# Performance work log

Hardware: AMD Instinct MI355X
Metric: run time of the kernel (lower is better)

The kernel has to match this reference:

```python
import jax, jax.numpy as jnp
import numpy as np

B, S, D = 1, 2048, 4096
H, KV, HD = 32, 8, 128
C = 4096  # cache length
THETA = 1000000.0
NEG = -1e9


def setup_inputs() -> dict:
    key = jax.random.key(0)
    ks = jax.random.split(key, 8)
    std = 0.02
    x = jax.random.normal(ks[0], (B, S, D), jnp.float32)
    wq = jax.random.normal(ks[1], (H * HD, D), jnp.float32) * std
    wk = jax.random.normal(ks[2], (KV * HD, D), jnp.float32) * std
    wv = jax.random.normal(ks[3], (KV * HD, D), jnp.float32) * std
    wo = jax.random.normal(ks[4], (D, H * HD), jnp.float32) * std
    k_cache = jnp.zeros((B, KV, C, HD), jnp.float32)
    v_cache = jnp.zeros((B, KV, C, HD), jnp.float32)
    # rotary tables (real/imag of freqs_cis)
    inv_freq = 1.0 / (THETA ** (jnp.arange(0, HD, 2, dtype=jnp.float32) / HD))  # [HD/2]
    t = jnp.arange(C, dtype=jnp.float32)
    freqs = jnp.outer(t, inv_freq)  # [C, HD/2]
    cos, sin = jnp.cos(freqs), jnp.sin(freqs)
    # causal additive mask over cache positions
    mask = jnp.where(jnp.tril(jnp.ones((C, C), bool)), 0.0, NEG).astype(jnp.float32)
    storage_idx = jnp.arange(S, dtype=jnp.int32)
    return {"x": x, "wq": wq, "wk": wk, "wv": wv, "wo": wo,
            "k_cache": k_cache, "v_cache": v_cache,
            "cos": cos, "sin": sin, "mask": mask, "storage_idx": storage_idx}


def _rope(x, cos, sin):
    # x: [B, h, S, HD]; cos/sin: [S, HD/2] -> complex mult on interleaved pairs
    xr, xi = x[..., 0::2], x[..., 1::2]
    c = cos[None, None, :, :]
    s = sin[None, None, :, :]
    or_, oi_ = xr * c - xi * s, xr * s + xi * c
    return jnp.stack([or_, oi_], axis=-1).reshape(x.shape)


def reference(x, wq, wk, wv, wo, k_cache, v_cache, cos, sin, mask, storage_idx):
    bsz, seqlen, _ = x.shape
    xq = jnp.einsum('bsd,ed->bse', x, wq).reshape(bsz, seqlen, H, HD).transpose(0, 2, 1, 3)
    xk = jnp.einsum('bsd,ed->bse', x, wk).reshape(bsz, seqlen, KV, HD).transpose(0, 2, 1, 3)
    xv = jnp.einsum('bsd,ed->bse', x, wv).reshape(bsz, seqlen, KV, HD).transpose(0, 2, 1, 3)
    cos_g, sin_g = cos[storage_idx], sin[storage_idx]
    xq = _rope(xq, cos_g, sin_g)
    xk = _rope(xk, cos_g, sin_g)
    # scatter into KV cache at storage_idx along the position axis
    keys = k_cache.at[:, :, storage_idx, :].set(xk)
    values = v_cache.at[:, :, storage_idx, :].set(xv)
    # GQA: repeat kv heads (kv-head-major, matches expand+reshape)
    rep = H // KV
    keys = jnp.repeat(keys, rep, axis=1)      # [B, H, C, HD]
    values = jnp.repeat(values, rep, axis=1)  # [B, H, C, HD]
    scores = jnp.einsum('bhqd,bhkd->bhqk', xq, keys) / np.sqrt(HD)
    scores = scores + mask[storage_idx][None, None, :, :]
    attn = jax.nn.softmax(scores, axis=-1)
    out = jnp.einsum('bhqk,bhkd->bhqd', attn, values)
    out = out.transpose(0, 2, 1, 3).reshape(bsz, seqlen, H * HD)
    return jnp.einsum('bse,de->bsd', out, wo)
```

## Files before the change

kernel.cpp:

```cpp
#include <hip/hip_runtime.h>
#include <cstdint>
#include <cstddef>

#define S_LEN 2048
#define DM    4096
#define NH    32
#define NKV   8
#define HDIM  128
#define EQ    4096
#define EKV   1024
#define SC_LOG2E 0.1275325477889277f

typedef unsigned short u16;
typedef short bf16x8 __attribute__((ext_vector_type(8)));
typedef float f32x4  __attribute__((ext_vector_type(4)));

__device__ __forceinline__ u16 f2bf(float f) {
  union { float f; unsigned u; } v; v.f = f;
  unsigned r = v.u + 0x7FFFu + ((v.u >> 16) & 1u);
  return (u16)(r >> 16);
}
__device__ __forceinline__ float bf2f(u16 b) {
  union { unsigned u; float f; } v; v.u = ((unsigned)b) << 16;
  return v.f;
}
__device__ __forceinline__ void glds16(const void* g, void* l) {
  __builtin_amdgcn_global_load_lds((const __attribute__((address_space(1))) void*)g,
                                   (__attribute__((address_space(3))) void*)l, 16, 0, 0);
}

__global__ void cast_all(const float* __restrict__ x, const float* __restrict__ wq,
                         const float* __restrict__ wk, const float* __restrict__ wv,
                         const float* __restrict__ wo,
                         u16* __restrict__ xb, u16* __restrict__ wqb,
                         u16* __restrict__ wkb, u16* __restrict__ wvb,
                         u16* __restrict__ wob) {
  const size_t stride = (size_t)gridDim.x * blockDim.x;
  for (size_t u = (size_t)blockIdx.x * blockDim.x + threadIdx.x; u < 12582912u; u += stride) {
    const float* in; u16* outp; size_t i;
    if (u < 2097152u)      { in = x;  outp = xb;  i = u; }
    else if (u < 6291456u) { in = wq; outp = wqb; i = u - 2097152u; }
    else if (u < 7340032u) { in = wk; outp = wkb; i = u - 6291456u; }
    else if (u < 8388608u) { in = wv; outp = wvb; i = u - 7340032u; }
    else                   { in = wo; outp = wob; i = u - 8388608u; }
    float4 f = ((const float4*)in)[i];
    ushort4 b;
    b.x = f2bf(f.x); b.y = f2bf(f.y); b.z = f2bf(f.z); b.w = f2bf(f.w);
    ((ushort4*)outp)[i] = b;
  }
}

template<int UN>
__device__ __forceinline__ void stage_t(const u16* __restrict__ g, int ldg, int k0,
                                        u16* ldsp, int t) {
  const int wb = t & ~63;
#pragma unroll
  for (int j = 0; j < UN / 256; ++j) {
    const int U = j * 256 + t;
    const int row = U >> 3, u = U & 7;
    const int uu = u ^ (row & 7);
    glds16(g + (size_t)row * ldg + k0 + uu * 8, ldsp + (size_t)(j * 256 + wb) * 8);
  }
}

template<int NF, bool QKV3>
__global__ __launch_bounds__(256, 2)
void gemm2p(const u16* __restrict__ A, const u16* __restrict__ B,
            void* __restrict__ Cq, u16* __restrict__ Ck, u16* __restrict__ Cv,
            int K) {
  constexpr int BN = 64 * NF;
  constexpr int AT = 128 * 64;
  constexpr int BT = BN * 64;
  __shared__ u16 lds[2 * (AT + BT)];
  const int t = threadIdx.x;
  const int l = t & 63, lr = l & 15, lg = l >> 4;
  const int wid = t >> 6, wm = wid >> 1, wn = wid & 1;
  const int m0 = blockIdx.y * 128, n0 = blockIdx.x * BN;
  const int KT = K >> 6;

  const u16* Ab = A + (size_t)m0 * K;
  const u16* Bb = B + (size_t)n0 * K;

  f32x4 acc[4][2 * NF] = {};

  stage_t<1024>(Ab, K, 0, &lds[0], t);
  stage_t<BT / 8>(Bb, K, 0, &lds[2 * AT], t);
  __syncthreads();

  int cur = 0;
#pragma unroll 1
  for (int tau = 0; tau < KT; ++tau) {
    const int kn = (tau + 1 < KT ? tau + 1 : KT - 1) * 64;
    stage_t<1024>(Ab, K, kn, &lds[(cur ^ 1) * AT], t);
    stage_t<BT / 8>(Bb, K, kn, &lds[2 * AT + (cur ^ 1) * BT], t);

    const int aBase = cur * AT;
    const int bBase = 2 * AT + cur * BT;

    bf16x8 af[4][2];
#pragma unroll
    for (int mf = 0; mf < 4; ++mf)
#pragma unroll
      for (int kk = 0; kk < 2; ++kk) {
        const int row = wm * 64 + mf * 16 + lr;
        const int uu = ((kk * 4 + lg) ^ (row & 7)) * 8;
        af[mf][kk] = *(const bf16x8*)&lds[aBase + row * 64 + uu];
      }

#pragma unroll
    for (int n = 0; n < 2 * NF; ++n) {
      const int brow = wn * (32 * NF) + n * 16 + lr;
      const int u0 = ((0 * 4 + lg) ^ (brow & 7)) * 8;
      const int u1 = ((1 * 4 + lg) ^ (brow & 7)) * 8;
      bf16x8 b0 = *(const bf16x8*)&lds[bBase + brow * 64 + u0];
      bf16x8 b1 = *(const bf16x8*)&lds[bBase + brow * 64 + u1];
#pragma unroll
      for (int mf = 0; mf < 4; ++mf) {
        acc[mf][n] = __builtin_amdgcn_mfma_f32_16x16x32_bf16(af[mf][0], b0, acc[mf][n], 0, 0, 0);
        acc[mf][n] = __builtin_amdgcn_mfma_f32_16x16x32_bf16(af[mf][1], b1, acc[mf][n], 0, 0, 0);
      }
    }
    __syncthreads();
    cur ^= 1;
  }

#pragma unroll
  for (int mf = 0; mf < 4; ++mf) {
    const int row = m0 + wm * 64 + mf * 16 + lg * 4;
#pragma unroll
    for (int n = 0; n < 2 * NF; ++n) {
      const int gc = n0 + wn * (32 * NF) + n * 16 + lr;
#pragma unroll
      for (int r = 0; r < 4; ++r) {
        if constexpr (QKV3) {
          if (gc < 4096)
            ((u16*)Cq)[(size_t)(row + r) * 4096 + gc] = f2bf(acc[mf][n][r]);
          else if (gc < 5120)
            Ck[(size_t)(row + r) * 1024 + (gc - 4096)] = f2bf(acc[mf][n][r]);
          else
            Cv[(size_t)(row + r) * 1024 + (gc - 5120)] = f2bf(acc[mf][n][r]);
        } else {
          ((float*)Cq)[(size_t)(row + r) * 4096 + gc] = acc[mf][n][r];
        }
      }
    }
  }
}

__global__ void rope_all(u16* __restrict__ qd, u16* __restrict__ kd,
                         const float* __restrict__ cosb, const float* __restrict__ sinb,
                         const int* __restrict__ sidx) {
  const int u = blockIdx.x * blockDim.x + threadIdx.x;
  u16* base; int s, b;
  if (u < 1048576) {
    base = qd + (size_t)u * 8;
    s = u >> 9;
    b = u & 15;
  } else if (u < 1310720) {
    const int u2 = u - 1048576;
    base = kd + (size_t)u2 * 8;
    s = u2 >> 7;
    b = u2 & 15;
  } else return;
  const int pos = sidx[s];
  const float4 c  = *(const float4*)&cosb[pos * 64 + b * 4];
  const float4 sn = *(const float4*)&sinb[pos * 64 + b * 4];
  uint4 raw = *(uint4*)base;
  u16* pe = (u16*)&raw;
  const float cc[4] = {c.x, c.y, c.z, c.w};
  const float ss[4] = {sn.x, sn.y, sn.z, sn.w};
#pragma unroll
  for (int j = 0; j < 4; ++j) {
    const float xr = bf2f(pe[2 * j]), xi = bf2f(pe[2 * j + 1]);
    pe[2 * j]     = f2bf(xr * cc[j] - xi * ss[j]);
    pe[2 * j + 1] = f2bf(xr * ss[j] + xi * cc[j]);
  }
  *(uint4*)base = raw;
}

__global__ void transpose_v(const u16* __restrict__ v, u16* __restrict__ vt) {
  __shared__ u16 tile[32][33];
  const int tx = threadIdx.x, ty = threadIdx.y;
  const int c0 = blockIdx.x * 32, s0 = blockIdx.y * 32;
#pragma unroll
  for (int j = 0; j < 32; j += 8)
    tile[ty + j][tx] = v[(size_t)(s0 + ty + j) * EKV + c0 + tx];
  __syncthreads();
#pragma unroll
  for (int j = 0; j < 32; j += 8)
    vt[(size_t)(c0 + ty + j) * S_LEN + s0 + tx] = tile[tx][ty + j];
}

#define ATTN_STAGE(TK, BUF) { \
  const int kv0s = (TK) * 64; \
  _Pragma("unroll") \
  for (int hh = 0; hh < 4; ++hh) { \
    const int f = hh * 256 + t; \
    { const int row = f >> 4, uu = f & 15, us = uu ^ (row & 7); \
      glds16(&k[(size_t)(kv0s + row) * EKV + kvh * HDIM + us * 8], &lK[BUF][(hh * 256 + wb) * 8]); } \
    { const int row = f >> 3, uu = f & 7, us = uu ^ (row & 7); \
      glds16(&vt[(size_t)(kvh * HDIM + row) * S_LEN + kv0s + us * 8], &lV[BUF][(hh * 256 + wb) * 8]); } \
  } }

#define TILE_STEP(QA, O, MR, LR, Q0) { \
  f32x4 sc[4] = {}; \
  _Pragma("unroll") \
  for (int n = 0; n < 4; ++n) { \
    _Pragma("unroll") \
    for (int kc = 0; kc < 4; ++kc) { \
      const int row = n * 16 + lr; \
      const int us = (kc * 4 + lg) ^ (row & 7); \
      bf16x8 bk = *(const bf16x8*)&lKc[row * 128 + us * 8]; \
      sc[n] = __builtin_amdgcn_mfma_f32_16x16x32_bf16(QA[kc], bk, sc[n], 0, 0, 0); \
    } \
  } \
  _Pragma("unroll") \
  for (int n = 0; n < 4; ++n) { \
    const int kvc = kv0 + n * 16 + lr; \
    _Pragma("unroll") \
    for (int r = 0; r < 4; ++r) { \
      const int qr = (Q0) + lg * 4 + r; \
      const float vv = sc[n][r] * SC_LOG2E; \
      sc[n][r] = (kvc > qr) ? -1e30f : vv; \
    } \
  } \
  _Pragma("unroll") \
  for (int r = 0; r < 4; ++r) { \
    float v = fmaxf(fmaxf(sc[0][r], sc[1][r]), fmaxf(sc[2][r], sc[3][r])); \
    v = fmaxf(v, __shfl_xor(v, 1)); \
    v = fmaxf(v, __shfl_xor(v, 2)); \
    v = fmaxf(v, __shfl_xor(v, 4)); \
    v = fmaxf(v, __shfl_xor(v, 8)); \
    const float mn = fmaxf(MR[r], v); \
    const float sf = __builtin_amdgcn_exp2f(MR[r] - mn); \
    MR[r] = mn; \
    float rs = 0.f; \
    _Pragma("unroll") \
    for (int n = 0; n < 4; ++n) { \
      const float pv = __builtin_amdgcn_exp2f(sc[n][r] - mn); \
      sc[n][r] = pv; \
      rs += pv; \
    } \
    rs += __shfl_xor(rs, 1); \
    rs += __shfl_xor(rs, 2); \
    rs += __shfl_xor(rs, 4); \
    rs += __shfl_xor(rs, 8); \
    LR[r] = LR[r] * sf + rs; \
    _Pragma("unroll") \
    for (int nh = 0; nh < 8; ++nh) O[nh][r] *= sf; \
  } \
  _Pragma("unroll") \
  for (int n = 0; n < 4; ++n) \
    _Pragma("unroll") \
    for (int r = 0; r < 4; ++r) \
      lPw[(lg * 4 + r) * 72 + n * 16 + lr] = f2bf(sc[n][r]); \
  _Pragma("unroll") \
  for (int kc2 = 0; kc2 < 2; ++kc2) { \
    bf16x8 pa = *(const bf16x8*)&lPw[lr * 72 + kc2 * 32 + lg * 8]; \
    _Pragma("unroll") \
    for (int nh = 0; nh < 8; ++nh) { \
      const int row = nh * 16 + lr; \
      const int us = (kc2 * 4 + lg) ^ (row & 7); \
      bf16x8 bv = *(const bf16x8*)&lVc[row * 64 + us * 8]; \
      O[nh] = __builtin_amdgcn_mfma_f32_16x16x32_bf16(pa, bv, O[nh], 0, 0, 0); \
    } \
  } }

__global__ __launch_bounds__(256, 2)
void attn_fwd(const u16* __restrict__ q, const u16* __restrict__ k,
              const u16* __restrict__ vt, u16* __restrict__ ao) {
  __shared__ u16 lK[2][64 * 128];
  __shared__ u16 lV[2][128 * 64];
  __shared__ u16 lP[4 * 16 * 72];
  const int t = threadIdx.x, w = t >> 6, l = t & 63;
  const int lr = l & 15, lg = l >> 4;
  const int wb = t & ~63;
  const int p = blockIdx.x, h = blockIdx.y;
  const int kvh = h >> 2;
  u16* lPw = &lP[w * (16 * 72)];

  const int q0A = p * 64 + w * 16;
  const int q0B = (31 - p) * 64 + w * 16;
  const int nt = 32 - p;

  bf16x8 qaA[4], qaB[4];
#pragma unroll
  for (int kc = 0; kc < 4; ++kc) {
    qaA[kc] = *(const bf16x8*)&q[(size_t)(q0A + lr) * EQ + h * HDIM + kc * 32 + lg * 8];
    qaB[kc] = *(const bf16x8*)&q[(size_t)(q0B + lr) * EQ + h * HDIM + kc * 32 + lg * 8];
  }

  f32x4 oA[8] = {}, oB[8] = {};
  float mA[4], lA[4], mB[4], lB[4];
#pragma unroll
  for (int r = 0; r < 4; ++r) { mA[r] = -1e30f; lA[r] = 0.f; mB[r] = -1e30f; lB[r] = 0.f; }

  int cur = 0;
  ATTN_STAGE(0, 0);
  __syncthreads();

#pragma unroll 1
  for (int tk = 0; tk < nt; ++tk) {
    const int kv0 = tk * 64;
    if (tk + 1 < nt) ATTN_STAGE(tk + 1, cur ^ 1);
    const u16* lKc = lK[cur];
    const u16* lVc = lV[cur];

    TILE_STEP(qaB, oB, mB, lB, q0B);
    if (tk <= p) {
      TILE_STEP(qaA, oA, mA, lA, q0A);
    }
    __syncthreads();
    cur ^= 1;
  }

#pragma unroll
  for (int nh = 0; nh < 8; ++nh)
#pragma unroll
    for (int r = 0; r < 4; ++r) {
      const int col = h * HDIM + nh * 16 + lr;
      ao[(size_t)(q0A + lg * 4 + r) * EQ + col] = f2bf(oA[nh][r] / lA[r]);
      ao[(size_t)(q0B + lg * 4 + r) * EQ + col] = f2bf(oB[nh][r] / lB[r]);
    }
}

extern "C" void kernel_launch(void* const* d_in, const int* in_sizes, int n_in,
                              void* d_out, int out_size, void* d_ws, size_t ws_size,
                              hipStream_t stream) {
  (void)in_sizes; (void)n_in; (void)out_size; (void)ws_size;
  const float* x    = (const float*)d_in[0];
  const float* wq   = (const float*)d_in[1];
  const float* wk   = (const float*)d_in[2];
  const float* wv   = (const float*)d_in[3];
  const float* wo   = (const float*)d_in[4];
  const float* cosb = (const float*)d_in[7];
  const float* sinb = (const float*)d_in[8];
  const int*   sidx = (const int*)d_in[10];
  float* out = (float*)d_out;

  u16* ws  = (u16*)d_ws;
  u16* xb  = ws;
  u16* wqb = xb  + (size_t)S_LEN * DM;
  u16* wkb = wqb + (size_t)EQ * DM;
  u16* wvb = wkb + (size_t)EKV * DM;
  u16* wob = wvb + (size_t)EKV * DM;
  u16* qb  = wob + (size_t)DM * EQ;
  u16* kb  = qb  + (size_t)S_LEN * EQ;
  u16* vb  = kb  + (size_t)S_LEN * EKV;
  u16* vtb = vb  + (size_t)S_LEN * EKV;
  u16* aob = vtb + (size_t)S_LEN * EKV;

  cast_all<<<2048, 256, 0, stream>>>(x, wq, wk, wv, wo, xb, wqb, wkb, wvb, wob);
  gemm2p<3, true><<<dim3(32, 16), 256, 0, stream>>>(xb, wqb, qb, kb, vb, DM);
  rope_all<<<5120, 256, 0, stream>>>(qb, kb, cosb, sinb, sidx);
  transpose_v<<<dim3(EKV / 32, S_LEN / 32), dim3(32, 8), 0, stream>>>(vb, vtb);
  attn_fwd<<<dim3(16, NH), 256, 0, stream>>>(qb, kb, vtb, aob);
  gemm2p<2, false><<<dim3(32, 16), 256, 0, stream>>>(aob, wob, out, nullptr, nullptr, EQ);
}
```

Measured before the change: 320.7 us.

## Fuse weight bf16 conversion into GEMM loads and share K fragments in attention

Drops the separate cast pass over all four weight matrices. Each GEMM now loads fp32 weight tiles into registers one step ahead, packs them to bf16 with v_cvt_pk_bf16_f32, and writes them into swizzled LDS; only the activation x is still cast up front. This removes a large read-then-write of the weights, but every row-block now re-reads fp32 weights, which doubles B-side traffic per tile and adds register pressure under the 2-blocks-per-SM launch bound. Separately, the attention loop loads each K fragment once and issues the score MFMAs for both query tiles together, cutting repeated LDS reads.

```diff
diff --git a/kernel.cpp b/kernel.cpp
--- a/kernel.cpp
+++ b/kernel.cpp
@@ -24,29 +24,23 @@
   union { unsigned u; float f; } v; v.u = ((unsigned)b) << 16;
   return v.f;
 }
+__device__ __forceinline__ unsigned cvt2bf(float lo, float hi) {
+  unsigned r;
+  asm("v_cvt_pk_bf16_f32 %0, %1, %2" : "=v"(r) : "v"(lo), "v"(hi));
+  return r;
+}
 __device__ __forceinline__ void glds16(const void* g, void* l) {
   __builtin_amdgcn_global_load_lds((const __attribute__((address_space(1))) void*)g,
                                    (__attribute__((address_space(3))) void*)l, 16, 0, 0);
 }
 
-__global__ void cast_all(const float* __restrict__ x, const float* __restrict__ wq,
-                         const float* __restrict__ wk, const float* __restrict__ wv,
-                         const float* __restrict__ wo,
-                         u16* __restrict__ xb, u16* __restrict__ wqb,
-                         u16* __restrict__ wkb, u16* __restrict__ wvb,
-                         u16* __restrict__ wob) {
+__global__ void cast_x(const float* __restrict__ x, u16* __restrict__ xb) {
   const size_t stride = (size_t)gridDim.x * blockDim.x;
-  for (size_t u = (size_t)blockIdx.x * blockDim.x + threadIdx.x; u < 12582912u; u += stride) {
-    const float* in; u16* outp; size_t i;
-    if (u < 2097152u)      { in = x;  outp = xb;  i = u; }
-    else if (u < 6291456u) { in = wq; outp = wqb; i = u - 2097152u; }
-    else if (u < 7340032u) { in = wk; outp = wkb; i = u - 6291456u; }
-    else if (u < 8388608u) { in = wv; outp = wvb; i = u - 7340032u; }
-    else                   { in = wo; outp = wob; i = u - 8388608u; }
-    float4 f = ((const float4*)in)[i];
+  for (size_t i = (size_t)blockIdx.x * blockDim.x + threadIdx.x; i < 2097152u; i += stride) {
+    float4 f = ((const float4*)x)[i];
     ushort4 b;
     b.x = f2bf(f.x); b.y = f2bf(f.y); b.z = f2bf(f.z); b.w = f2bf(f.w);
-    ((ushort4*)outp)[i] = b;
+    ((ushort4*)xb)[i] = b;
   }
 }
 
@@ -65,12 +59,15 @@
 
 template<int NF, bool QKV3>
 __global__ __launch_bounds__(256, 2)
-void gemm2p(const u16* __restrict__ A, const u16* __restrict__ B,
+void gemm2p(const u16* __restrict__ A,
+            const float* __restrict__ Bq, const float* __restrict__ Bk,
+            const float* __restrict__ Bv,
             void* __restrict__ Cq, u16* __restrict__ Ck, u16* __restrict__ Cv,
             int K) {
   constexpr int BN = 64 * NF;
   constexpr int AT = 128 * 64;
   constexpr int BT = BN * 64;
+  constexpr int NU = BN / 32;
   __shared__ u16 lds[2 * (AT + BT)];
   const int t = threadIdx.x;
   const int l = t & 63, lr = l & 15, lg = l >> 4;
@@ -79,20 +76,61 @@
   const int KT = K >> 6;
 
   const u16* Ab = A + (size_t)m0 * K;
-  const u16* Bb = B + (size_t)n0 * K;
+
+  const float* bptr[NU];
+  int bswz[NU];
+#pragma unroll
+  for (int j = 0; j < NU; ++j) {
+    const int U = j * 256 + t;
+    const int brow = U >> 3, u = U & 7;
+    const int gr = n0 + brow;
+    const float* bp;
+    if constexpr (QKV3) {
+      if (gr < 4096)      bp = Bq + (size_t)gr * K;
+      else if (gr < 5120) bp = Bk + (size_t)(gr - 4096) * K;
+      else                bp = Bv + (size_t)(gr - 5120) * K;
+    } else {
+      bp = Bq + (size_t)gr * K;
+    }
+    bptr[j] = bp + u * 8;
+    bswz[j] = brow * 64 + (u ^ (brow & 7)) * 8;
+  }
+
+  float4 blo[NU], bhi[NU];
+#define LOADB(KT_IDX) { \
+  const int k0_ = (KT_IDX) * 64; \
+  _Pragma("unroll") \
+  for (int j = 0; j < NU; ++j) { \
+    blo[j] = *(const float4*)&bptr[j][k0_]; \
+    bhi[j] = *(const float4*)&bptr[j][k0_ + 4]; \
+  } }
+#define WRITEB(BUF) { \
+  _Pragma("unroll") \
+  for (int j = 0; j < NU; ++j) { \
+    uint4 pk; \
+    pk.x = cvt2bf(blo[j].x, blo[j].y); \
+    pk.y = cvt2bf(blo[j].z, blo[j].w); \
+    pk.z = cvt2bf(bhi[j].x, bhi[j].y); \
+    pk.w = cvt2bf(bhi[j].z, bhi[j].w); \
+    *(uint4*)&lds[2 * AT + (BUF) * BT + bswz[j]] = pk; \
+  } }
 
   f32x4 acc[4][2 * NF] = {};
 
+  LOADB(0);
   stage_t<1024>(Ab, K, 0, &lds[0], t);
-  stage_t<BT / 8>(Bb, K, 0, &lds[2 * AT], t);
+  WRITEB(0);
+  LOADB(KT > 1 ? 1 : 0);
   __syncthreads();
 
   int cur = 0;
 #pragma unroll 1
   for (int tau = 0; tau < KT; ++tau) {
-    const int kn = (tau + 1 < KT ? tau + 1 : KT - 1) * 64;
-    stage_t<1024>(Ab, K, kn, &lds[(cur ^ 1) * AT], t);
-    stage_t<BT / 8>(Bb, K, kn, &lds[2 * AT + (cur ^ 1) * BT], t);
+    const int nxt = (tau + 1 < KT ? tau + 1 : KT - 1);
+    const int nx2 = (tau + 2 < KT ? tau + 2 : KT - 1);
+    WRITEB(cur ^ 1);
+    stage_t<1024>(Ab, K, nxt * 64, &lds[(cur ^ 1) * AT], t);
+    LOADB(nx2);
 
     const int aBase = cur * AT;
     const int bBase = 2 * AT + cur * BT;
@@ -145,6 +183,8 @@
       }
     }
   }
+#undef LOADB
+#undef WRITEB
 }
 
 __global__ void rope_all(u16* __restrict__ qd, u16* __restrict__ kd,
@@ -202,31 +242,20 @@
       glds16(&vt[(size_t)(kvh * HDIM + row) * S_LEN + kv0s + us * 8], &lV[BUF][(hh * 256 + wb) * 8]); } \
   } }
 
-#define TILE_STEP(QA, O, MR, LR, Q0) { \
-  f32x4 sc[4] = {}; \
-  _Pragma("unroll") \
-  for (int n = 0; n < 4; ++n) { \
-    _Pragma("unroll") \
-    for (int kc = 0; kc < 4; ++kc) { \
-      const int row = n * 16 + lr; \
-      const int us = (kc * 4 + lg) ^ (row & 7); \
-      bf16x8 bk = *(const bf16x8*)&lKc[row * 128 + us * 8]; \
-      sc[n] = __builtin_amdgcn_mfma_f32_16x16x32_bf16(QA[kc], bk, sc[n], 0, 0, 0); \
-    } \
-  } \
+#define SMPV(SC, O, MR, LR, Q0) { \
   _Pragma("unroll") \
   for (int n = 0; n < 4; ++n) { \
     const int kvc = kv0 + n * 16 + lr; \
     _Pragma("unroll") \
     for (int r = 0; r < 4; ++r) { \
       const int qr = (Q0) + lg * 4 + r; \
-      const float vv = sc[n][r] * SC_LOG2E; \
-      sc[n][r] = (kvc > qr) ? -1e30f : vv; \
+      const float vv = SC[n][r] * SC_LOG2E; \
+      SC[n][r] = (kvc > qr) ? -1e30f : vv; \
     } \
   } \
   _Pragma("unroll") \
   for (int r = 0; r < 4; ++r) { \
-    float v = fmaxf(fmaxf(sc[0][r], sc[1][r]), fmaxf(sc[2][r], sc[3][r])); \
+    float v = fmaxf(fmaxf(SC[0][r], SC[1][r]), fmaxf(SC[2][r], SC[3][r])); \
     v = fmaxf(v, __shfl_xor(v, 1)); \
     v = fmaxf(v, __shfl_xor(v, 2)); \
     v = fmaxf(v, __shfl_xor(v, 4)); \
@@ -237,8 +266,8 @@
     float rs = 0.f; \
     _Pragma("unroll") \
     for (int n = 0; n < 4; ++n) { \
-      const float pv = __builtin_amdgcn_exp2f(sc[n][r] - mn); \
-      sc[n][r] = pv; \
+      const float pv = __builtin_amdgcn_exp2f(SC[n][r] - mn); \
+      SC[n][r] = pv; \
       rs += pv; \
     } \
     rs += __shfl_xor(rs, 1); \
@@ -253,7 +282,7 @@
   for (int n = 0; n < 4; ++n) \
     _Pragma("unroll") \
     for (int r = 0; r < 4; ++r) \
-      lPw[(lg * 4 + r) * 72 + n * 16 + lr] = f2bf(sc[n][r]); \
+      lPw[(lg * 4 + r) * 72 + n * 16 + lr] = f2bf(SC[n][r]); \
   _Pragma("unroll") \
   for (int kc2 = 0; kc2 < 2; ++kc2) { \
     bf16x8 pa = *(const bf16x8*)&lPw[lr * 72 + kc2 * 32 + lg * 8]; \
@@ -306,9 +335,34 @@
     const u16* lKc = lK[cur];
     const u16* lVc = lV[cur];
 
-    TILE_STEP(qaB, oB, mB, lB, q0B);
     if (tk <= p) {
-      TILE_STEP(qaA, oA, mA, lA, q0A);
+      f32x4 scB[4] = {}, scA[4] = {};
+#pragma unroll
+      for (int n = 0; n < 4; ++n) {
+#pragma unroll
+        for (int kc = 0; kc < 4; ++kc) {
+          const int row = n * 16 + lr;
+          const int us = (kc * 4 + lg) ^ (row & 7);
+          bf16x8 bk = *(const bf16x8*)&lKc[row * 128 + us * 8];
+          scB[n] = __builtin_amdgcn_mfma_f32_16x16x32_bf16(qaB[kc], bk, scB[n], 0, 0, 0);
+          scA[n] = __builtin_amdgcn_mfma_f32_16x16x32_bf16(qaA[kc], bk, scA[n], 0, 0, 0);
+        }
+      }
+      SMPV(scB, oB, mB, lB, q0B);
+      SMPV(scA, oA, mA, lA, q0A);
+    } else {
+      f32x4 scB[4] = {};
+#pragma unroll
+      for (int n = 0; n < 4; ++n) {
+#pragma unroll
+        for (int kc = 0; kc < 4; ++kc) {
+          const int row = n * 16 + lr;
+          const int us = (kc * 4 + lg) ^ (row & 7);
+          bf16x8 bk = *(const bf16x8*)&lKc[row * 128 + us * 8];
+          scB[n] = __builtin_amdgcn_mfma_f32_16x16x32_bf16(qaB[kc], bk, scB[n], 0, 0, 0);
+        }
+      }
+      SMPV(scB, oB, mB, lB, q0B);
     }
     __syncthreads();
     cur ^= 1;
@@ -340,20 +394,16 @@
 
   u16* ws  = (u16*)d_ws;
   u16* xb  = ws;
-  u16* wqb = xb  + (size_t)S_LEN * DM;
-  u16* wkb = wqb + (size_t)EQ * DM;
-  u16* wvb = wkb + (size_t)EKV * DM;
-  u16* wob = wvb + (size_t)EKV * DM;
-  u16* qb  = wob + (size_t)DM * EQ;
+  u16* qb  = xb  + (size_t)S_LEN * DM;
   u16* kb  = qb  + (size_t)S_LEN * EQ;
   u16* vb  = kb  + (size_t)S_LEN * EKV;
   u16* vtb = vb  + (size_t)S_LEN * EKV;
   u16* aob = vtb + (size_t)S_LEN * EKV;
 
-  cast_all<<<2048, 256, 0, stream>>>(x, wq, wk, wv, wo, xb, wqb, wkb, wvb, wob);
-  gemm2p<3, true><<<dim3(32, 16), 256, 0, stream>>>(xb, wqb, qb, kb, vb, DM);
+  cast_x<<<1024, 256, 0, stream>>>(x, xb);
+  gemm2p<3, true><<<dim3(32, 16), 256, 0, stream>>>(xb, wq, wk, wv, qb, kb, vb, DM);
   rope_all<<<5120, 256, 0, stream>>>(qb, kb, cosb, sinb, sidx);
   transpose_v<<<dim3(EKV / 32, S_LEN / 32), dim3(32, 8), 0, stream>>>(vb, vtb);
   attn_fwd<<<dim3(16, NH), 256, 0, stream>>>(qb, kb, vtb, aob);
-  gemm2p<2, false><<<dim3(32, 16), 256, 0, stream>>>(aob, wob, out, nullptr, nullptr, EQ);
-}
+  gemm2p<2, false><<<dim3(32, 16), 256, 0, stream>>>(aob, wo, nullptr, nullptr, out, nullptr, nullptr, EQ);
+}
```

Result: slower. 373.0 us (+16.3%).

## Swap QK^T MFMA operands so softmax rows live per lane in attention

Applied to the files above, without the earlier changes.

Computes S^T by swapping the MFMA operand order, which puts each query row's scores across one lane's registers. The row max and row sum then need only two cross-lane shuffles instead of four per row. The P tile is written with packed bf16 conversion (v_cvt_pk_bf16_f32) as 8-byte stores instead of scalar 2-byte stores. The two query tiles now share each K fragment load via interleaved MFMAs. In exchange, the per-row rescale factors and final normalizers must be broadcast back to the output layout with __shfl.

```diff
diff --git a/kernel.cpp b/kernel.cpp
--- a/kernel.cpp
+++ b/kernel.cpp
@@ -23,6 +23,11 @@
 __device__ __forceinline__ float bf2f(u16 b) {
   union { unsigned u; float f; } v; v.u = ((unsigned)b) << 16;
   return v.f;
+}
+__device__ __forceinline__ unsigned cvt2bf(float a, float b) {
+  unsigned r;
+  asm("v_cvt_pk_bf16_f32 %0, %1, %2" : "=v"(r) : "v"(a), "v"(b));
+  return r;
 }
 __device__ __forceinline__ void glds16(const void* g, void* l) {
   __builtin_amdgcn_global_load_lds((const __attribute__((address_space(1))) void*)g,
@@ -202,58 +207,56 @@
       glds16(&vt[(size_t)(kvh * HDIM + row) * S_LEN + kv0s + us * 8], &lV[BUF][(hh * 256 + wb) * 8]); } \
   } }
 
-#define TILE_STEP(QA, O, MR, LR, Q0) { \
-  f32x4 sc[4] = {}; \
+#define SMPV_SW(SC, O, MR, LR, Q0) { \
   _Pragma("unroll") \
   for (int n = 0; n < 4; ++n) { \
     _Pragma("unroll") \
-    for (int kc = 0; kc < 4; ++kc) { \
-      const int row = n * 16 + lr; \
-      const int us = (kc * 4 + lg) ^ (row & 7); \
-      bf16x8 bk = *(const bf16x8*)&lKc[row * 128 + us * 8]; \
-      sc[n] = __builtin_amdgcn_mfma_f32_16x16x32_bf16(QA[kc], bk, sc[n], 0, 0, 0); \
+    for (int r = 0; r < 4; ++r) { \
+      const int kvc = kv0 + n * 16 + lg * 4 + r; \
+      const int qr = (Q0) + lr; \
+      const float vv = SC[n][r] * SC_LOG2E; \
+      SC[n][r] = (kvc > qr) ? -1e30f : vv; \
     } \
   } \
-  _Pragma("unroll") \
-  for (int n = 0; n < 4; ++n) { \
-    const int kvc = kv0 + n * 16 + lr; \
+  float vmx = SC[0][0]; \
+  _Pragma("unroll") \
+  for (int n = 0; n < 4; ++n) \
+    _Pragma("unroll") \
+    for (int r = 0; r < 4; ++r) vmx = fmaxf(vmx, SC[n][r]); \
+  vmx = fmaxf(vmx, __shfl_xor(vmx, 16)); \
+  vmx = fmaxf(vmx, __shfl_xor(vmx, 32)); \
+  const float mn = fmaxf(MR, vmx); \
+  const float sf = __builtin_amdgcn_exp2f(MR - mn); \
+  MR = mn; \
+  float rs = 0.f; \
+  _Pragma("unroll") \
+  for (int n = 0; n < 4; ++n) \
     _Pragma("unroll") \
     for (int r = 0; r < 4; ++r) { \
-      const int qr = (Q0) + lg * 4 + r; \
-      const float vv = sc[n][r] * SC_LOG2E; \
-      sc[n][r] = (kvc > qr) ? -1e30f : vv; \
+      const float pv = __builtin_amdgcn_exp2f(SC[n][r] - mn); \
+      SC[n][r] = pv; \
+      rs += pv; \
+    } \
+  rs += __shfl_xor(rs, 16); \
+  rs += __shfl_xor(rs, 32); \
+  LR = LR * sf + rs; \
+  { \
+    const float s0 = __shfl(sf, lg * 4 + 0); \
+    const float s1 = __shfl(sf, lg * 4 + 1); \
+    const float s2 = __shfl(sf, lg * 4 + 2); \
+    const float s3 = __shfl(sf, lg * 4 + 3); \
+    _Pragma("unroll") \
+    for (int nh = 0; nh < 8; ++nh) { \
+      O[nh][0] *= s0; O[nh][1] *= s1; O[nh][2] *= s2; O[nh][3] *= s3; \
     } \
   } \
   _Pragma("unroll") \
-  for (int r = 0; r < 4; ++r) { \
-    float v = fmaxf(fmaxf(sc[0][r], sc[1][r]), fmaxf(sc[2][r], sc[3][r])); \
-    v = fmaxf(v, __shfl_xor(v, 1)); \
-    v = fmaxf(v, __shfl_xor(v, 2)); \
-    v = fmaxf(v, __shfl_xor(v, 4)); \
-    v = fmaxf(v, __shfl_xor(v, 8)); \
-    const float mn = fmaxf(MR[r], v); \
-    const float sf = __builtin_amdgcn_exp2f(MR[r] - mn); \
-    MR[r] = mn; \
-    float rs = 0.f; \
-    _Pragma("unroll") \
-    for (int n = 0; n < 4; ++n) { \
-      const float pv = __builtin_amdgcn_exp2f(sc[n][r] - mn); \
-      sc[n][r] = pv; \
-      rs += pv; \
-    } \
-    rs += __shfl_xor(rs, 1); \
-    rs += __shfl_xor(rs, 2); \
-    rs += __shfl_xor(rs, 4); \
-    rs += __shfl_xor(rs, 8); \
-    LR[r] = LR[r] * sf + rs; \
-    _Pragma("unroll") \
-    for (int nh = 0; nh < 8; ++nh) O[nh][r] *= sf; \
+  for (int n = 0; n < 4; ++n) { \
+    uint2 wpk; \
+    wpk.x = cvt2bf(SC[n][0], SC[n][1]); \
+    wpk.y = cvt2bf(SC[n][2], SC[n][3]); \
+    *(uint2*)&lPw[lr * 72 + n * 16 + lg * 4] = wpk; \
   } \
-  _Pragma("unroll") \
-  for (int n = 0; n < 4; ++n) \
-    _Pragma("unroll") \
-    for (int r = 0; r < 4; ++r) \
-      lPw[(lg * 4 + r) * 72 + n * 16 + lr] = f2bf(sc[n][r]); \
   _Pragma("unroll") \
   for (int kc2 = 0; kc2 < 2; ++kc2) { \
     bf16x8 pa = *(const bf16x8*)&lPw[lr * 72 + kc2 * 32 + lg * 8]; \
@@ -291,9 +294,7 @@
   }
 
   f32x4 oA[8] = {}, oB[8] = {};
-  float mA[4], lA[4], mB[4], lB[4];
-#pragma unroll
-  for (int r = 0; r < 4; ++r) { mA[r] = -1e30f; lA[r] = 0.f; mB[r] = -1e30f; lB[r] = 0.f; }
+  float mA = -1e30f, lA = 0.f, mB = -1e30f, lB = 0.f;
 
   int cur = 0;
   ATTN_STAGE(0, 0);
@@ -306,22 +307,55 @@
     const u16* lKc = lK[cur];
     const u16* lVc = lV[cur];
 
-    TILE_STEP(qaB, oB, mB, lB, q0B);
     if (tk <= p) {
-      TILE_STEP(qaA, oA, mA, lA, q0A);
+      f32x4 scB[4] = {}, scA[4] = {};
+#pragma unroll
+      for (int n = 0; n < 4; ++n) {
+#pragma unroll
+        for (int kc = 0; kc < 4; ++kc) {
+          const int row = n * 16 + lr;
+          const int us = (kc * 4 + lg) ^ (row & 7);
+          bf16x8 bk = *(const bf16x8*)&lKc[row * 128 + us * 8];
+          scB[n] = __builtin_amdgcn_mfma_f32_16x16x32_bf16(bk, qaB[kc], scB[n], 0, 0, 0);
+          scA[n] = __builtin_amdgcn_mfma_f32_16x16x32_bf16(bk, qaA[kc], scA[n], 0, 0, 0);
+        }
+      }
+      SMPV_SW(scB, oB, mB, lB, q0B);
+      SMPV_SW(scA, oA, mA, lA, q0A);
+    } else {
+      f32x4 scB[4] = {};
+#pragma unroll
+      for (int n = 0; n < 4; ++n) {
+#pragma unroll
+        for (int kc = 0; kc < 4; ++kc) {
+          const int row = n * 16 + lr;
+          const int us = (kc * 4 + lg) ^ (row & 7);
+          bf16x8 bk = *(const bf16x8*)&lKc[row * 128 + us * 8];
+          scB[n] = __builtin_amdgcn_mfma_f32_16x16x32_bf16(bk, qaB[kc], scB[n], 0, 0, 0);
+        }
+      }
+      SMPV_SW(scB, oB, mB, lB, q0B);
     }
     __syncthreads();
     cur ^= 1;
   }
 
-#pragma unroll
-  for (int nh = 0; nh < 8; ++nh)
-#pragma unroll
-    for (int r = 0; r < 4; ++r) {
-      const int col = h * HDIM + nh * 16 + lr;
-      ao[(size_t)(q0A + lg * 4 + r) * EQ + col] = f2bf(oA[nh][r] / lA[r]);
-      ao[(size_t)(q0B + lg * 4 + r) * EQ + col] = f2bf(oB[nh][r] / lB[r]);
-    }
+  {
+    const float lA0 = __shfl(lA, lg * 4 + 0), lA1 = __shfl(lA, lg * 4 + 1);
+    const float lA2 = __shfl(lA, lg * 4 + 2), lA3 = __shfl(lA, lg * 4 + 3);
+    const float lB0 = __shfl(lB, lg * 4 + 0), lB1 = __shfl(lB, lg * 4 + 1);
+    const float lB2 = __shfl(lB, lg * 4 + 2), lB3 = __shfl(lB, lg * 4 + 3);
+    const float rlA[4] = {lA0, lA1, lA2, lA3};
+    const float rlB[4] = {lB0, lB1, lB2, lB3};
+#pragma unroll
+    for (int nh = 0; nh < 8; ++nh)
+#pragma unroll
+      for (int r = 0; r < 4; ++r) {
+        const int col = h * HDIM + nh * 16 + lr;
+        ao[(size_t)(q0A + lg * 4 + r) * EQ + col] = f2bf(oA[nh][r] / rlA[r]);
+        ao[(size_t)(q0B + lg * 4 + r) * EQ + col] = f2bf(oB[nh][r] / rlB[r]);
+      }
+  }
 }
 
 extern "C" void kernel_launch(void* const* d_in, const int* in_sizes, int n_in,
```

Measured after the change: 387.7 us. 1.21x slower.

## Triple-buffer GEMM with K=32 stages and fine-grained waits; interleave attention QK MFMAs

Applied to the files above, without the earlier changes.

The GEMM kernel moves from a double-buffered K=64 LDS pipeline to a triple-buffered K=32 pipeline. It uses explicit vmcnt/lgkmcnt waits, raw s_barrier, sched barriers and setprio around the MFMA block so global loads run further ahead of compute. The attention kernel computes the QK^T MFMAs for both query tiles in one loop sharing each K fragment load, then runs softmax and PV separately. The hand-counted vmcnt values depend on the exact number of outstanding loads, and the extra LDS buffer may affect occupancy.

```diff
diff --git a/kernel.cpp b/kernel.cpp
--- a/kernel.cpp
+++ b/kernel.cpp
@@ -50,78 +50,93 @@
   }
 }
 
-template<int UN>
-__device__ __forceinline__ void stage_t(const u16* __restrict__ g, int ldg, int k0,
-                                        u16* ldsp, int t) {
-  const int wb = t & ~63;
-#pragma unroll
-  for (int j = 0; j < UN / 256; ++j) {
-    const int U = j * 256 + t;
-    const int row = U >> 3, u = U & 7;
-    const int uu = u ^ (row & 7);
-    glds16(g + (size_t)row * ldg + k0 + uu * 8, ldsp + (size_t)(j * 256 + wb) * 8);
-  }
-}
-
 template<int NF, bool QKV3>
 __global__ __launch_bounds__(256, 2)
-void gemm2p(const u16* __restrict__ A, const u16* __restrict__ B,
+void gemm3b(const u16* __restrict__ A, const u16* __restrict__ B,
             void* __restrict__ Cq, u16* __restrict__ Ck, u16* __restrict__ Cv,
             int K) {
-  constexpr int BN = 64 * NF;
-  constexpr int AT = 128 * 64;
-  constexpr int BT = BN * 64;
-  __shared__ u16 lds[2 * (AT + BT)];
+  constexpr int BN  = 64 * NF;
+  constexpr int AT  = 128 * 32;
+  constexpr int BT  = BN * 32;
+  constexpr int BUFS = AT + BT;
+  constexpr int BJ  = BT / 8 / 256;
+  __shared__ u16 lds[3 * BUFS];
   const int t = threadIdx.x;
   const int l = t & 63, lr = l & 15, lg = l >> 4;
   const int wid = t >> 6, wm = wid >> 1, wn = wid & 1;
   const int m0 = blockIdx.y * 128, n0 = blockIdx.x * BN;
-  const int KT = K >> 6;
+  const int KT = K >> 5;
+  const int wb = t & ~63;
 
   const u16* Ab = A + (size_t)m0 * K;
   const u16* Bb = B + (size_t)n0 * K;
 
+#define STAGE3(TAU, BI) { \
+  const int k0_ = (TAU) * 32; \
+  u16* base_ = &lds[(BI) * BUFS]; \
+  _Pragma("unroll") \
+  for (int j = 0; j < 2; ++j) { \
+    const int U = j * 256 + t; \
+    const int row = U >> 2, u = U & 3; \
+    const int us = u ^ ((row ^ (row >> 2)) & 3); \
+    glds16(Ab + (size_t)row * K + k0_ + us * 8, base_ + (j * 256 + wb) * 8); \
+  } \
+  _Pragma("unroll") \
+  for (int j = 0; j < BJ; ++j) { \
+    const int U = j * 256 + t; \
+    const int row = U >> 2, u = U & 3; \
+    const int us = u ^ ((row ^ (row >> 2)) & 3); \
+    glds16(Bb + (size_t)row * K + k0_ + us * 8, base_ + AT + (j * 256 + wb) * 8); \
+  } }
+
   f32x4 acc[4][2 * NF] = {};
 
-  stage_t<1024>(Ab, K, 0, &lds[0], t);
-  stage_t<BT / 8>(Bb, K, 0, &lds[2 * AT], t);
-  __syncthreads();
+  STAGE3(0, 0);
+  STAGE3(1, 1);
+  STAGE3(2, 2);
+  if constexpr (NF == 3) asm volatile("s_waitcnt vmcnt(10)" ::: "memory");
+  else                   asm volatile("s_waitcnt vmcnt(8)" ::: "memory");
+  __builtin_amdgcn_sched_barrier(0);
+  __builtin_amdgcn_s_barrier();
 
   int cur = 0;
 #pragma unroll 1
   for (int tau = 0; tau < KT; ++tau) {
-    const int kn = (tau + 1 < KT ? tau + 1 : KT - 1) * 64;
-    stage_t<1024>(Ab, K, kn, &lds[(cur ^ 1) * AT], t);
-    stage_t<BT / 8>(Bb, K, kn, &lds[2 * AT + (cur ^ 1) * BT], t);
-
-    const int aBase = cur * AT;
-    const int bBase = 2 * AT + cur * BT;
-
-    bf16x8 af[4][2];
+    const u16* bufp = &lds[cur * BUFS];
+
+    bf16x8 af[4], bfr[2 * NF];
+#pragma unroll
+    for (int mf = 0; mf < 4; ++mf) {
+      const int row = wm * 64 + mf * 16 + lr;
+      const int us = (lg ^ ((row ^ (row >> 2)) & 3)) * 8;
+      af[mf] = *(const bf16x8*)&bufp[row * 32 + us];
+    }
+#pragma unroll
+    for (int n = 0; n < 2 * NF; ++n) {
+      const int row = wn * (32 * NF) + n * 16 + lr;
+      const int us = (lg ^ ((row ^ (row >> 2)) & 3)) * 8;
+      bfr[n] = *(const bf16x8*)&bufp[AT + row * 32 + us];
+    }
+    asm volatile("s_waitcnt lgkmcnt(0)" ::: "memory");
+    __builtin_amdgcn_sched_barrier(0);
+    __builtin_amdgcn_s_barrier();
+
+    const int ts = (tau + 3 < KT) ? tau + 3 : KT - 1;
+    STAGE3(ts, cur);
+
+    __builtin_amdgcn_s_setprio(1);
 #pragma unroll
     for (int mf = 0; mf < 4; ++mf)
 #pragma unroll
-      for (int kk = 0; kk < 2; ++kk) {
-        const int row = wm * 64 + mf * 16 + lr;
-        const int uu = ((kk * 4 + lg) ^ (row & 7)) * 8;
-        af[mf][kk] = *(const bf16x8*)&lds[aBase + row * 64 + uu];
-      }
-
-#pragma unroll
-    for (int n = 0; n < 2 * NF; ++n) {
-      const int brow = wn * (32 * NF) + n * 16 + lr;
-      const int u0 = ((0 * 4 + lg) ^ (brow & 7)) * 8;
-      const int u1 = ((1 * 4 + lg) ^ (brow & 7)) * 8;
-      bf16x8 b0 = *(const bf16x8*)&lds[bBase + brow * 64 + u0];
-      bf16x8 b1 = *(const bf16x8*)&lds[bBase + brow * 64 + u1];
-#pragma unroll
-      for (int mf = 0; mf < 4; ++mf) {
-        acc[mf][n] = __builtin_amdgcn_mfma_f32_16x16x32_bf16(af[mf][0], b0, acc[mf][n], 0, 0, 0);
-        acc[mf][n] = __builtin_amdgcn_mfma_f32_16x16x32_bf16(af[mf][1], b1, acc[mf][n], 0, 0, 0);
-      }
-    }
-    __syncthreads();
-    cur ^= 1;
+      for (int n = 0; n < 2 * NF; ++n)
+        acc[mf][n] = __builtin_amdgcn_mfma_f32_16x16x32_bf16(af[mf], bfr[n], acc[mf][n], 0, 0, 0);
+    __builtin_amdgcn_s_setprio(0);
+
+    if constexpr (NF == 3) asm volatile("s_waitcnt vmcnt(5)" ::: "memory");
+    else                   asm volatile("s_waitcnt vmcnt(4)" ::: "memory");
+    __builtin_amdgcn_sched_barrier(0);
+    __builtin_amdgcn_s_barrier();
+    cur = (cur == 2) ? 0 : cur + 1;
   }
 
 #pragma unroll
@@ -145,6 +160,7 @@
       }
     }
   }
+#undef STAGE3
 }
 
 __global__ void rope_all(u16* __restrict__ qd, u16* __restrict__ kd,
@@ -202,31 +218,20 @@
       glds16(&vt[(size_t)(kvh * HDIM + row) * S_LEN + kv0s + us * 8], &lV[BUF][(hh * 256 + wb) * 8]); } \
   } }
 
-#define TILE_STEP(QA, O, MR, LR, Q0) { \
-  f32x4 sc[4] = {}; \
+#define SMPV(SC, O, MR, LR, Q0) { \
   _Pragma("unroll") \
   for (int n = 0; n < 4; ++n) { \
-    _Pragma("unroll") \
-    for (int kc = 0; kc < 4; ++kc) { \
-      const int row = n * 16 + lr; \
-      const int us = (kc * 4 + lg) ^ (row & 7); \
-      bf16x8 bk = *(const bf16x8*)&lKc[row * 128 + us * 8]; \
-      sc[n] = __builtin_amdgcn_mfma_f32_16x16x32_bf16(QA[kc], bk, sc[n], 0, 0, 0); \
+    const int kvc = kv0 + n * 16 + lr; \
+    _Pragma("unroll") \
+    for (int r = 0; r < 4; ++r) { \
+      const int qr = (Q0) + lg * 4 + r; \
+      const float vv = SC[n][r] * SC_LOG2E; \
+      SC[n][r] = (kvc > qr) ? -1e30f : vv; \
     } \
   } \
   _Pragma("unroll") \
-  for (int n = 0; n < 4; ++n) { \
-    const int kvc = kv0 + n * 16 + lr; \
-    _Pragma("unroll") \
-    for (int r = 0; r < 4; ++r) { \
-      const int qr = (Q0) + lg * 4 + r; \
-      const float vv = sc[n][r] * SC_LOG2E; \
-      sc[n][r] = (kvc > qr) ? -1e30f : vv; \
-    } \
-  } \
-  _Pragma("unroll") \
   for (int r = 0; r < 4; ++r) { \
-    float v = fmaxf(fmaxf(sc[0][r], sc[1][r]), fmaxf(sc[2][r], sc[3][r])); \
+    float v = fmaxf(fmaxf(SC[0][r], SC[1][r]), fmaxf(SC[2][r], SC[3][r])); \
     v = fmaxf(v, __shfl_xor(v, 1)); \
     v = fmaxf(v, __shfl_xor(v, 2)); \
     v = fmaxf(v, __shfl_xor(v, 4)); \
@@ -237,8 +242,8 @@
     float rs = 0.f; \
     _Pragma("unroll") \
     for (int n = 0; n < 4; ++n) { \
-      const float pv = __builtin_amdgcn_exp2f(sc[n][r] - mn); \
-      sc[n][r] = pv; \
+      const float pv = __builtin_amdgcn_exp2f(SC[n][r] - mn); \
+      SC[n][r] = pv; \
       rs += pv; \
     } \
     rs += __shfl_xor(rs, 1); \
@@ -253,7 +258,7 @@
   for (int n = 0; n < 4; ++n) \
     _Pragma("unroll") \
     for (int r = 0; r < 4; ++r) \
-      lPw[(lg * 4 + r) * 72 + n * 16 + lr] = f2bf(sc[n][r]); \
+      lPw[(lg * 4 + r) * 72 + n * 16 + lr] = f2bf(SC[n][r]); \
   _Pragma("unroll") \
   for (int kc2 = 0; kc2 < 2; ++kc2) { \
     bf16x8 pa = *(const bf16x8*)&lPw[lr * 72 + kc2 * 32 + lg * 8]; \
@@ -306,9 +311,34 @@
     const u16* lKc = lK[cur];
     const u16* lVc = lV[cur];
 
-    TILE_STEP(qaB, oB, mB, lB, q0B);
     if (tk <= p) {
-      TILE_STEP(qaA, oA, mA, lA, q0A);
+      f32x4 scB[4] = {}, scA[4] = {};
+#pragma unroll
+      for (int n = 0; n < 4; ++n) {
+#pragma unroll
+        for (int kc = 0; kc < 4; ++kc) {
+          const int row = n * 16 + lr;
+          const int us = (kc * 4 + lg) ^ (row & 7);
+          bf16x8 bk = *(const bf16x8*)&lKc[row * 128 + us * 8];
+          scB[n] = __builtin_amdgcn_mfma_f32_16x16x32_bf16(qaB[kc], bk, scB[n], 0, 0, 0);
+          scA[n] = __builtin_amdgcn_mfma_f32_16x16x32_bf16(qaA[kc], bk, scA[n], 0, 0, 0);
+        }
+      }
+      SMPV(scB, oB, mB, lB, q0B);
+      SMPV(scA, oA, mA, lA, q0A);
+    } else {
+      f32x4 scB[4] = {};
+#pragma unroll
+      for (int n = 0; n < 4; ++n) {
+#pragma unroll
+        for (int kc = 0; kc < 4; ++kc) {
+          const int row = n * 16 + lr;
+          const int us = (kc * 4 + lg) ^ (row & 7);
+          bf16x8 bk = *(const bf16x8*)&lKc[row * 128 + us * 8];
+          scB[n] = __builtin_amdgcn_mfma_f32_16x16x32_bf16(qaB[kc], bk, scB[n], 0, 0, 0);
+        }
+      }
+      SMPV(scB, oB, mB, lB, q0B);
     }
     __syncthreads();
     cur ^= 1;
@@ -351,9 +381,9 @@
   u16* aob = vtb + (size_t)S_LEN * EKV;
 
   cast_all<<<2048, 256, 0, stream>>>(x, wq, wk, wv, wo, xb, wqb, wkb, wvb, wob);
-  gemm2p<3, true><<<dim3(32, 16), 256, 0, stream>>>(xb, wqb, qb, kb, vb, DM);
+  gemm3b<3, true><<<dim3(32, 16), 256, 0, stream>>>(xb, wqb, qb, kb, vb, DM);
   rope_all<<<5120, 256, 0, stream>>>(qb, kb, cosb, sinb, sidx);
   transpose_v<<<dim3(EKV / 32, S_LEN / 32), dim3(32, 8), 0, stream>>>(vb, vtb);
   attn_fwd<<<dim3(16, NH), 256, 0, stream>>>(qb, kb, vtb, aob);
-  gemm2p<2, false><<<dim3(32, 16), 256, 0, stream>>>(aob, wob, out, nullptr, nullptr, EQ);
-}
+  gemm3b<2, false><<<dim3(32, 16), 256, 0, stream>>>(aob, wob, out, nullptr, nullptr, EQ);
+}
```

Result: slower. 361.2 us (+12.6%).
